# Kernel tuning notes

Measured on AMD Instinct MI355X. Metric: run time of the kernel, lower is better.

The kernel has to match this reference:

```python
import math
import jax, jax.numpy as jnp
import numpy as np

CLUSTER_RATIO1 = 0.0625
CLUSTER_RATIO2 = 0.35
K_LAYER1 = 8
K_LAYER2 = 3


def _dpc_knn(x, cluster_num, k, key):
    """Density-peak clustering with KNN density. x: [B,N,C] -> idx_cluster [B,N]."""
    B, N, C = x.shape
    sq = jnp.sum(x * x, axis=-1)  # [B,N]
    d2 = sq[:, :, None] + sq[:, None, :] - 2.0 * jnp.einsum('bnc,bmc->bnm', x, x)
    dist = jnp.sqrt(jnp.maximum(d2, 0.0)) / jnp.sqrt(jnp.asarray(C, x.dtype))  # cdist / C**0.5
    # k nearest (smallest) distances
    neg_dn, _ = jax.lax.top_k(-dist, k)
    dist_nearest = -neg_dn  # [B,N,k]
    density = jnp.exp(-jnp.mean(dist_nearest ** 2, axis=-1))
    density = density + jax.random.uniform(key, density.shape, dtype=density.dtype) * 1e-6
    mask = (density[:, None, :] > density[:, :, None]).astype(x.dtype)  # [B,N,N]
    dist_max = jnp.max(dist.reshape(B, -1), axis=-1)[:, None, None]
    parent_dist = jnp.min(dist * mask + dist_max * (1.0 - mask), axis=-1)  # [B,N]
    score = parent_dist * density
    _, index_down = jax.lax.top_k(score, cluster_num)  # [B,cluster_num] cluster centers
    # assign each token to nearest center
    dm = jnp.take_along_axis(dist, index_down[:, :, None], axis=1)  # [B,cluster_num,N]
    idx_cluster = jnp.argmin(dm, axis=1)  # [B,N]
    bidx = jnp.arange(B)[:, None]
    idx_cluster = idx_cluster.at[bidx, index_down].set(
        jnp.broadcast_to(jnp.arange(cluster_num)[None, :], index_down.shape))
    return idx_cluster


def _merge_tokens(x, idx_cluster, cluster_num):
    """Weighted (uniform) scatter-mean of tokens into clusters. x: [B,N,C]."""
    B, N, C = x.shape
    flat = (idx_cluster + jnp.arange(B)[:, None] * cluster_num).reshape(-1)  # [B*N]
    ones = jnp.ones((B * N,), x.dtype)
    all_w = jax.ops.segment_sum(ones, flat, num_segments=B * cluster_num) + 1e-6
    norm_w = 1.0 / all_w[flat]  # token_weight == 1
    merged = jax.ops.segment_sum(x.reshape(B * N, C) * norm_w[:, None], flat,
                                 num_segments=B * cluster_num)
    return merged.reshape(B, cluster_num, C)


def _group(meta1, meta2, idx_cluster2, score_w, score_b):
    """Reorder [meta2[v]; members of cluster v from meta1] per cluster, scaled by modulation."""
    T, K1, C = meta1.shape
    K2 = meta2.shape[1]
    modu = jax.nn.softmax(meta2.mean(axis=2) @ score_w.T + score_b, axis=-1)  # [T,K2]
    # composite sort key: (cluster_id, 0 for meta2 center, 1+i for meta1 member i) -> stable grouping
    cid = jnp.concatenate([jnp.broadcast_to(jnp.arange(K2)[None, :], (T, K2)),
                           idx_cluster2], axis=1)  # [T,K2+K1]
    pos = jnp.concatenate([jnp.zeros((T, K2), jnp.int32),
                           jnp.broadcast_to(jnp.arange(1, K1 + 1, dtype=jnp.int32)[None, :], (T, K1))],
                          axis=1)
    sort_key = cid * (K1 + 2) + pos
    order = jnp.argsort(sort_key, axis=1)  # stable; keys are unique anyway
    tokens = jnp.concatenate([meta2, meta1], axis=1)  # [T,K2+K1,C]
    sorted_tokens = jnp.take_along_axis(tokens, order[:, :, None], axis=1)
    sorted_cid = jnp.take_along_axis(cid, order, axis=1)
    scale = jnp.take_along_axis(modu, sorted_cid, axis=1)  # [T,K2+K1]
    return sorted_tokens * scale[:, :, None]


def setup_inputs() -> dict:
    key = jax.random.key(0)
    k1, k2, k3 = jax.random.split(key, 3)
    T, N, C = 128, 256, 1408
    vis_embed = jax.random.normal(k1, (T, N, C), dtype=jnp.float32)
    score_w = jax.random.normal(k2, (6, 6), dtype=jnp.float32) * 0.1
    score_b = jax.random.normal(k3, (6,), dtype=jnp.float32) * 0.1
    return {"vis_embed": vis_embed, "score_w": score_w, "score_b": score_b}


def reference(vis_embed, score_w, score_b):
    T, N, C = vis_embed.shape
    cn1 = max(math.ceil(N * CLUSTER_RATIO1), 1)      # 16
    cn2 = max(math.ceil(cn1 * CLUSTER_RATIO2), 1)    # 6
    nk = jax.random.split(jax.random.key(42), 2)
    idx1 = _dpc_knn(vis_embed, cn1, K_LAYER1, nk[0])
    meta1 = _merge_tokens(vis_embed, idx1, cn1)       # [T,16,C]
    idx2 = _dpc_knn(meta1, cn2, K_LAYER2, nk[1])
    meta2 = _merge_tokens(meta1, idx2, cn2)           # [T,6,C]
    return _group(meta1, meta2, idx2, score_w, score_b)  # [T,22,C]
```

## Files before the change

kernel.cpp:

```cpp
#include <hip/hip_runtime.h>
#include <math.h>

#define T_BATCH 128
#define N_TOK   256
#define C_DIM   1408
#define CN1     16
#define KNN1    8
#define CN2     6
#define KNN2    3
#define NOUT    22
#define LSTR    40

typedef __attribute__((ext_vector_type(4))) short sh4;
typedef __attribute__((ext_vector_type(8))) short sh8;
typedef __attribute__((ext_vector_type(4))) float f32x4;

union frag_u { sh4 h[2]; sh8 v; };

__device__ inline sh8 ld_frag(const short* p) {
    frag_u u;
    u.h[0] = *(const sh4*)p;
    u.h[1] = *(const sh4*)(p + 4);
    return u.v;
}

__device__ inline void split2(float v0, float v1, unsigned& hip, unsigned& lop) {
    unsigned u0 = __float_as_uint(v0);
    unsigned u1 = __float_as_uint(v1);
    hip = (u0 >> 16) | (u1 & 0xFFFF0000u);
    float l0 = v0 - __uint_as_float(u0 & 0xFFFF0000u);
    float l1 = v1 - __uint_as_float(u1 & 0xFFFF0000u);
    unsigned w0 = __float_as_uint(l0);
    unsigned w1 = __float_as_uint(l1);
    w0 = w0 + 0x7FFFu + ((w0 >> 16) & 1u);
    w1 = w1 + 0x7FFFu + ((w1 >> 16) & 1u);
    lop = (w0 >> 16) | (w1 & 0xFFFF0000u);
}

__global__ __launch_bounds__(256, 3) void gemm_dist_mfma(const float* __restrict__ x,
                                                         float* __restrict__ dist) {
    const int t  = blockIdx.z;
    const int i0 = blockIdx.x * 128;
    const int j0 = blockIdx.y * 128;
    const bool diag = (i0 == j0);
    const float* X = x + (size_t)t * N_TOK * C_DIM;

    __shared__ short Ahi[128 * LSTR], Alo[128 * LSTR], Bhi[128 * LSTR], Blo[128 * LSTR];
    __shared__ float nredA[256], nredB[256];
    __shared__ float snA[128], snB[128];

    const int tid  = threadIdx.x;
    const int wave = tid >> 6;
    const int lane = tid & 63;
    const int qr   = wave >> 1;
    const int qc   = wave & 1;
    const int srow = tid >> 1;
    const int scol = (tid & 1) * 16;
    const int fr   = lane & 15;
    const int fq   = lane >> 4;

    const short* BhiS = diag ? Ahi : Bhi;
    const short* BloS = diag ? Alo : Blo;

    f32x4 acc[4][4];
#pragma unroll
    for (int a = 0; a < 4; a++)
#pragma unroll
        for (int b = 0; b < 4; b++) acc[a][b] = (f32x4){0.f, 0.f, 0.f, 0.f};

    const float* Arow = X + (size_t)(i0 + srow) * C_DIM + scol;
    const float* Brow = X + (size_t)(j0 + srow) * C_DIM + scol;
    float nA = 0.f, nB = 0.f;

    for (int k0 = 0; k0 < C_DIM; k0 += 32) {
        float av[16], bv[16];
#pragma unroll
        for (int g = 0; g < 4; g++) {
            float4 a = *(const float4*)(Arow + k0 + g * 4);
            av[g * 4 + 0] = a.x; av[g * 4 + 1] = a.y; av[g * 4 + 2] = a.z; av[g * 4 + 3] = a.w;
        }
#pragma unroll
        for (int e = 0; e < 16; e++) nA += av[e] * av[e];
        if (!diag) {
#pragma unroll
            for (int g = 0; g < 4; g++) {
                float4 b = *(const float4*)(Brow + k0 + g * 4);
                bv[g * 4 + 0] = b.x; bv[g * 4 + 1] = b.y; bv[g * 4 + 2] = b.z; bv[g * 4 + 3] = b.w;
            }
#pragma unroll
            for (int e = 0; e < 16; e++) nB += bv[e] * bv[e];
        }

        unsigned ah[8], al[8], bh[8], bl[8];
#pragma unroll
        for (int p = 0; p < 8; p++) split2(av[2 * p], av[2 * p + 1], ah[p], al[p]);
        if (!diag) {
#pragma unroll
            for (int p = 0; p < 8; p++) split2(bv[2 * p], bv[2 * p + 1], bh[p], bl[p]);
        }
        __syncthreads();
        unsigned* AhiW = (unsigned*)&Ahi[srow * LSTR + scol];
        unsigned* AloW = (unsigned*)&Alo[srow * LSTR + scol];
#pragma unroll
        for (int p = 0; p < 8; p++) { AhiW[p] = ah[p]; AloW[p] = al[p]; }
        if (!diag) {
            unsigned* BhiW = (unsigned*)&Bhi[srow * LSTR + scol];
            unsigned* BloW = (unsigned*)&Blo[srow * LSTR + scol];
#pragma unroll
            for (int p = 0; p < 8; p++) { BhiW[p] = bh[p]; BloW[p] = bl[p]; }
        }
        __syncthreads();

        sh8 fAh[4], fAl[4], fBh[4], fBl[4];
#pragma unroll
        for (int mt = 0; mt < 4; mt++) {
            int ro = (qr * 64 + mt * 16 + fr) * LSTR + fq * 8;
            fAh[mt] = ld_frag(&Ahi[ro]);
            fAl[mt] = ld_frag(&Alo[ro]);
            int co = (qc * 64 + mt * 16 + fr) * LSTR + fq * 8;
            fBh[mt] = ld_frag(&BhiS[co]);
            fBl[mt] = ld_frag(&BloS[co]);
        }
#pragma unroll
        for (int mt = 0; mt < 4; mt++)
#pragma unroll
            for (int nt = 0; nt < 4; nt++) {
                acc[mt][nt] = __builtin_amdgcn_mfma_f32_16x16x32_bf16(fAh[mt], fBh[nt], acc[mt][nt], 0, 0, 0);
                acc[mt][nt] = __builtin_amdgcn_mfma_f32_16x16x32_bf16(fAh[mt], fBl[nt], acc[mt][nt], 0, 0, 0);
                acc[mt][nt] = __builtin_amdgcn_mfma_f32_16x16x32_bf16(fAl[mt], fBh[nt], acc[mt][nt], 0, 0, 0);
            }
    }

    nredA[tid] = nA;
    nredB[tid] = diag ? nA : nB;
    __syncthreads();
    if (tid < 128) {
        snA[tid] = nredA[2 * tid] + nredA[2 * tid + 1];
        snB[tid] = nredB[2 * tid] + nredB[2 * tid + 1];
    }
    __syncthreads();

    const float inv_sqrtC = 1.0f / sqrtf((float)C_DIM);
    float* Dt = dist + (size_t)t * N_TOK * N_TOK;
#pragma unroll
    for (int mt = 0; mt < 4; mt++)
#pragma unroll
        for (int nt = 0; nt < 4; nt++) {
            int jl = qc * 64 + nt * 16 + fr;
            float sqj = snB[jl];
            int jg = j0 + jl;
#pragma unroll
            for (int r = 0; r < 4; r++) {
                int il = qr * 64 + mt * 16 + fq * 4 + r;
                int ig = i0 + il;
                float d2 = snA[il] + sqj - 2.0f * acc[mt][nt][r];
                float v = (ig == jg) ? 0.0f : sqrtf(fmaxf(d2, 0.0f)) * inv_sqrtC;
                Dt[(size_t)ig * N_TOK + jg] = v;
            }
        }
}

__global__ __launch_bounds__(256) void dpc1_fused(const float* __restrict__ dist,
                                                  int* __restrict__ memb,
                                                  int* __restrict__ cntg,
                                                  int* __restrict__ offg) {
    const int t   = blockIdx.x;
    const int tid = threadIdx.x;
    const float* D = dist + (size_t)t * N_TOK * N_TOK;

    __shared__ float dens_s[N_TOK];
    __shared__ float red[N_TOK];
    __shared__ unsigned long long wbest[4];
    __shared__ int centers[CN1];
    __shared__ int bks[N_TOK];
    __shared__ int cnt_s[CN1], off_s[CN1];

    float m[KNN1];
#pragma unroll
    for (int q = 0; q < KNN1; q++) m[q] = 3.4e38f;
    float mx = 0.f;
#pragma unroll 8
    for (int j = 0; j < N_TOK; j++) {
        float d = D[(size_t)j * N_TOK + tid];
        mx = fmaxf(mx, d);
        float xv = d;
#pragma unroll
        for (int q = 0; q < KNN1; q++) {
            float lo = fminf(m[q], xv);
            xv = fmaxf(m[q], xv);
            m[q] = lo;
        }
    }
    float s2 = 0.f;
#pragma unroll
    for (int q = 0; q < KNN1; q++) s2 += m[q] * m[q];
    float dens = expf(-s2 / (float)KNN1);
    dens_s[tid] = dens;
    red[tid] = mx;
    __syncthreads();
#pragma unroll
    for (int s = 128; s > 0; s >>= 1) {
        if (tid < s) red[tid] = fmaxf(red[tid], red[tid + s]);
        __syncthreads();
    }
    float dmax = red[0];

    float pd = dmax;
#pragma unroll 8
    for (int j = 0; j < N_TOK; j++) {
        float d = D[(size_t)j * N_TOK + tid];
        float dj = dens_s[j];
        pd = (dj > dens) ? fminf(pd, d) : pd;
    }
    float score = pd * dens;

    unsigned long long key = ((unsigned long long)__float_as_uint(score) << 32)
                           | (unsigned)(65535 - tid);
    for (int k = 0; k < CN1; k++) {
        unsigned long long mm = key;
#pragma unroll
        for (int off = 32; off > 0; off >>= 1) {
            unsigned long long o = __shfl_xor(mm, off);
            mm = (o > mm) ? o : mm;
        }
        if ((tid & 63) == 0) wbest[tid >> 6] = mm;
        __syncthreads();
        unsigned long long b = wbest[0];
#pragma unroll
        for (int w = 1; w < 4; w++) b = (wbest[w] > b) ? wbest[w] : b;
        int idx = 65535 - (int)(b & 0xFFFFull);
        if (tid == 0) centers[k] = idx;
        if (tid == idx) key = 0;
        __syncthreads();
    }

    float bd = 3.4e38f; int bk = 0;
#pragma unroll
    for (int k = 0; k < CN1; k++) {
        float d = D[(size_t)centers[k] * N_TOK + tid];
        if (d < bd) { bd = d; bk = k; }
    }
#pragma unroll
    for (int k = 0; k < CN1; k++) if (tid == centers[k]) bk = k;

    bks[tid] = bk;
    __syncthreads();
    if (tid < CN1) {
        int c = 0;
        for (int j = 0; j < N_TOK; j++) c += (bks[j] == tid);
        cnt_s[tid] = c;
    }
    __syncthreads();
    if (tid == 0) {
        int o = 0;
        for (int q = 0; q < CN1; q++) { off_s[q] = o; o += cnt_s[q]; }
    }
    __syncthreads();
    int rank = 0;
    for (int j = 0; j < tid; j++) rank += (bks[j] == bk);
    memb[t * N_TOK + off_s[bk] + rank] = tid;
    if (tid < CN1) {
        cntg[t * CN1 + tid] = cnt_s[tid];
        offg[t * CN1 + tid] = off_s[tid];
    }
}

__global__ __launch_bounds__(256) void merge1_kernel(const float* __restrict__ x,
                                                     const int* __restrict__ memb,
                                                     const int* __restrict__ cntg,
                                                     const int* __restrict__ offg,
                                                     float* __restrict__ meta1) {
    const int q   = blockIdx.x;
    const int t   = blockIdx.y;
    const int tid = threadIdx.x;
    const int n    = cntg[t * CN1 + q];
    const int base = t * N_TOK + offg[t * CN1 + q];
    const int c0 = tid, c1 = tid + 256;
    const bool act1 = (c1 < C_DIM / 4);

    float a0x = 0.f, a0y = 0.f, a0z = 0.f, a0w = 0.f;
    float a1x = 0.f, a1y = 0.f, a1z = 0.f, a1w = 0.f;
    for (int m = 0; m < n; m++) {
        int row = memb[base + m];
        const float4* xr = (const float4*)(x + ((size_t)t * N_TOK + row) * C_DIM);
        float4 v0 = xr[c0];
        a0x += v0.x; a0y += v0.y; a0z += v0.z; a0w += v0.w;
        if (act1) {
            float4 v1 = xr[c1];
            a1x += v1.x; a1y += v1.y; a1z += v1.z; a1w += v1.w;
        }
    }
    float w = 1.0f / ((float)n + 1e-6f);
    float4* mr = (float4*)(meta1 + ((size_t)t * CN1 + q) * C_DIM);
    float4 o0; o0.x = a0x * w; o0.y = a0y * w; o0.z = a0z * w; o0.w = a0w * w;
    mr[c0] = o0;
    if (act1) {
        float4 o1; o1.x = a1x * w; o1.y = a1y * w; o1.z = a1z * w; o1.w = a1w * w;
        mr[c1] = o1;
    }
}

__global__ __launch_bounds__(256) void layer2_kernel(const float* __restrict__ meta1,
                                                     const float* __restrict__ score_w,
                                                     const float* __restrict__ score_b,
                                                     float* __restrict__ out) {
    const int t   = blockIdx.x;
    const int tid = threadIdx.x;
    const float* M = meta1 + (size_t)t * CN1 * C_DIM;

    __shared__ float buf[CN1][132];
    __shared__ float d2s[CN1][CN1];
    __shared__ float m2[CN2][C_DIM];
    __shared__ float dens[CN1], scor[CN1], nrm[CN1], rmx[CN1];
    __shared__ int   centers[CN2], idx2s[CN1], cnt2[CN2];
    __shared__ float modu[CN2], msum[CN2];
    __shared__ int   srcRow[NOUT], cidArr[NOUT];
    __shared__ float dmax_sh;

    const int ti = tid >> 4;
    const int tj = tid & 15;

    float acc = 0.f;
    for (int c0 = 0; c0 < C_DIM; c0 += 128) {
        for (int e = tid; e < CN1 * 128; e += 256) {
            int r = e >> 7, c = e & 127;
            buf[r][c] = M[(size_t)r * C_DIM + c0 + c];
        }
        __syncthreads();
#pragma unroll
        for (int cc = 0; cc < 128; cc += 4) {
            float4 a = *(const float4*)&buf[ti][cc];
            float4 b = *(const float4*)&buf[tj][cc];
            acc += a.x * b.x + a.y * b.y + a.z * b.z + a.w * b.w;
        }
        __syncthreads();
    }
    if (ti == tj) nrm[ti] = acc;
    __syncthreads();

    const float inv_sqrtC = 1.0f / sqrtf((float)C_DIM);
    {
        float d2 = nrm[ti] + nrm[tj] - 2.f * acc;
        d2s[ti][tj] = sqrtf(fmaxf(d2, 0.f)) * inv_sqrtC;
    }
    __syncthreads();

    if (tid < CN1) {
        float m0 = 3.4e38f, m1 = 3.4e38f, m2v = 3.4e38f, mx = 0.f;
        for (int j = 0; j < CN1; j++) {
            float d = d2s[tid][j];
            mx = fmaxf(mx, d);
            if (d < m2v) {
                m2v = d;
                if (m2v < m1) { float tmp = m2v; m2v = m1; m1 = tmp; }
                if (m1 < m0)  { float tmp = m1;  m1 = m0;  m0 = tmp; }
            }
        }
        dens[tid] = expf(-(m0 * m0 + m1 * m1 + m2v * m2v) / (float)KNN2);
        rmx[tid] = mx;
    }
    __syncthreads();
    if (tid == 0) {
        float g = 0.f;
        for (int j = 0; j < CN1; j++) g = fmaxf(g, rmx[j]);
        dmax_sh = g;
    }
    __syncthreads();

    if (tid < CN1) {
        float di = dens[tid];
        float pd = dmax_sh;
        for (int j = 0; j < CN1; j++)
            if (dens[j] > di) pd = fminf(pd, d2s[tid][j]);
        scor[tid] = pd * di;
    }
    __syncthreads();

    if (tid == 0) {
        for (int k = 0; k < CN2; k++) {
            float best = -3.4e38f; int bi = 0;
            for (int j = 0; j < CN1; j++)
                if (scor[j] > best) { best = scor[j]; bi = j; }
            centers[k] = bi;
            scor[bi] = -3.4e38f;
        }
    }
    __syncthreads();

    if (tid < CN1) {
        float bd = 3.4e38f; int bk = 0;
#pragma unroll
        for (int k = 0; k < CN2; k++) {
            float d = d2s[centers[k]][tid];
            if (d < bd) { bd = d; bk = k; }
        }
#pragma unroll
        for (int k = 0; k < CN2; k++) if (tid == centers[k]) bk = k;
        idx2s[tid] = bk;
    }
    __syncthreads();

    if (tid == 0) {
        for (int v = 0; v < CN2; v++) cnt2[v] = 0;
        for (int i = 0; i < CN1; i++) cnt2[idx2s[i]]++;
        int slot = 0;
        for (int v = 0; v < CN2; v++) {
            srcRow[slot] = CN1 + v; cidArr[slot] = v; slot++;
            for (int i = 0; i < CN1; i++)
                if (idx2s[i] == v) { srcRow[slot] = i; cidArr[slot] = v; slot++; }
        }
        for (int v = 0; v < CN2; v++) msum[v] = 0.f;
    }
    __syncthreads();

    float ls[CN2] = {0.f, 0.f, 0.f, 0.f, 0.f, 0.f};
    for (int ch = tid; ch < C_DIM; ch += 256) {
        float a6[CN2] = {0.f, 0.f, 0.f, 0.f, 0.f, 0.f};
        for (int r = 0; r < CN1; r++) {
            float v = M[(size_t)r * C_DIM + ch];
            int c = idx2s[r];
#pragma unroll
            for (int q = 0; q < CN2; q++) a6[q] += (c == q) ? v : 0.f;
        }
#pragma unroll
        for (int q = 0; q < CN2; q++) {
            float mv = a6[q] / ((float)cnt2[q] + 1e-6f);
            m2[q][ch] = mv;
            ls[q] += mv;
        }
    }
#pragma unroll
    for (int q = 0; q < CN2; q++) atomicAdd(&msum[q], ls[q]);
    __syncthreads();

    if (tid == 0) {
        float mean[CN2], lg[CN2];
        for (int v = 0; v < CN2; v++) mean[v] = msum[v] / (float)C_DIM;
        float mxl = -3.4e38f;
        for (int u = 0; u < CN2; u++) {
            float s = score_b[u];
            for (int v = 0; v < CN2; v++) s += mean[v] * score_w[u * CN2 + v];
            lg[u] = s;
            mxl = fmaxf(mxl, s);
        }
        float den = 0.f;
        for (int u = 0; u < CN2; u++) { lg[u] = expf(lg[u] - mxl); den += lg[u]; }
        for (int u = 0; u < CN2; u++) modu[u] = lg[u] / den;
    }
    __syncthreads();

    float* ob = out + (size_t)t * NOUT * C_DIM;
    for (int ch = tid; ch < C_DIM; ch += 256) {
#pragma unroll
        for (int s = 0; s < NOUT; s++) {
            int r = srcRow[s];
            float v = (r < CN1) ? M[(size_t)r * C_DIM + ch] : m2[r - CN1][ch];
            ob[(size_t)s * C_DIM + ch] = v * modu[cidArr[s]];
        }
    }
}

extern "C" void kernel_launch(void* const* d_in, const int* in_sizes, int n_in,
                              void* d_out, int out_size, void* d_ws, size_t ws_size,
                              hipStream_t stream) {
    const float* x  = (const float*)d_in[0];
    const float* sw = (const float*)d_in[1];
    const float* sb = (const float*)d_in[2];
    float* out = (float*)d_out;

    float* ws     = (float*)d_ws;
    float* dist   = ws;
    float* meta1  = dist + (size_t)T_BATCH * N_TOK * N_TOK;
    int*   memb   = (int*)(meta1 + (size_t)T_BATCH * CN1 * C_DIM);
    int*   cntg   = memb + (size_t)T_BATCH * N_TOK;
    int*   offg   = cntg + T_BATCH * CN1;

    gemm_dist_mfma<<<dim3(2, 2, T_BATCH), 256, 0, stream>>>(x, dist);
    dpc1_fused<<<T_BATCH, 256, 0, stream>>>(dist, memb, cntg, offg);
    merge1_kernel<<<dim3(CN1, T_BATCH), 256, 0, stream>>>(x, memb, cntg, offg, meta1);
    layer2_kernel<<<T_BATCH, 256, 0, stream>>>(meta1, sw, sb, out);
}
```

Before: 487.5 us.

## Exploit distance symmetry with 64x64 tiles and split KNN density across 512 threads

The distance GEMM moves from 128x128 tiles to 64x64 tiles and computes only the upper-triangular tile pairs (10 per batch), writing each result and its transpose. This cuts redundant MFMA work and gives more blocks for occupancy. The DPC kernel now uses 512 threads, with each half scanning half the rows and using four independent insertion lists for ILP, then merges the partial top-k lists and the parent-distance minima through shared memory. The risks are uncoalesced transposed float4 stores and extra shared memory and merge steps.

```diff
diff --git a/kernel.cpp b/kernel.cpp
--- a/kernel.cpp
+++ b/kernel.cpp
@@ -9,7 +9,7 @@
 #define CN2     6
 #define KNN2    3
 #define NOUT    22
-#define LSTR    40
+#define LS      44
 
 typedef __attribute__((ext_vector_type(4))) short sh4;
 typedef __attribute__((ext_vector_type(8))) short sh8;
@@ -37,185 +37,225 @@
     lop = (w0 >> 16) | (w1 & 0xFFFF0000u);
 }
 
-__global__ __launch_bounds__(256, 3) void gemm_dist_mfma(const float* __restrict__ x,
-                                                         float* __restrict__ dist) {
-    const int t  = blockIdx.z;
-    const int i0 = blockIdx.x * 128;
-    const int j0 = blockIdx.y * 128;
-    const bool diag = (i0 == j0);
+#define INS8(m, v) {                                   \
+    float _x = (v);                                    \
+    _Pragma("unroll")                                  \
+    for (int _q = 0; _q < 8; _q++) {                   \
+        float _lo = fminf(m[_q], _x);                  \
+        _x = fmaxf(m[_q], _x);                         \
+        m[_q] = _lo;                                   \
+    }                                                  \
+}
+
+__global__ __launch_bounds__(256, 4) void gemm_dist_sym(const float* __restrict__ x,
+                                                        float* __restrict__ dist) {
+    const int t = blockIdx.y;
+    const int p = blockIdx.x;
+    const int bi = (p < 4) ? 0 : (p < 7) ? 1 : (p < 9) ? 2 : 3;
+    const int bj = (p < 4) ? p : (p < 7) ? p - 3 : (p < 9) ? p - 5 : 3;
+    const int i0 = bi * 64, j0 = bj * 64;
+    const bool diag = (bi == bj);
     const float* X = x + (size_t)t * N_TOK * C_DIM;
 
-    __shared__ short Ahi[128 * LSTR], Alo[128 * LSTR], Bhi[128 * LSTR], Blo[128 * LSTR];
-    __shared__ float nredA[256], nredB[256];
-    __shared__ float snA[128], snB[128];
+    __shared__ short Ahi[64 * LS], Alo[64 * LS], Bhi[64 * LS], Blo[64 * LS];
+    __shared__ float nred[512];
+    __shared__ float snA[64], snB[64];
 
     const int tid  = threadIdx.x;
     const int wave = tid >> 6;
     const int lane = tid & 63;
     const int qr   = wave >> 1;
     const int qc   = wave & 1;
-    const int srow = tid >> 1;
-    const int scol = (tid & 1) * 16;
+    const int srow = tid >> 2;
+    const int sq   = tid & 3;
     const int fr   = lane & 15;
     const int fq   = lane >> 4;
 
     const short* BhiS = diag ? Ahi : Bhi;
     const short* BloS = diag ? Alo : Blo;
 
-    f32x4 acc[4][4];
-#pragma unroll
-    for (int a = 0; a < 4; a++)
-#pragma unroll
-        for (int b = 0; b < 4; b++) acc[a][b] = (f32x4){0.f, 0.f, 0.f, 0.f};
-
-    const float* Arow = X + (size_t)(i0 + srow) * C_DIM + scol;
-    const float* Brow = X + (size_t)(j0 + srow) * C_DIM + scol;
+    f32x4 acc[2][2];
+#pragma unroll
+    for (int a = 0; a < 2; a++)
+#pragma unroll
+        for (int b = 0; b < 2; b++) acc[a][b] = (f32x4){0.f, 0.f, 0.f, 0.f};
+
+    const float* Arow = X + (size_t)(i0 + srow) * C_DIM + sq * 8;
+    const float* Brow = X + (size_t)(j0 + srow) * C_DIM + sq * 8;
     float nA = 0.f, nB = 0.f;
 
     for (int k0 = 0; k0 < C_DIM; k0 += 32) {
-        float av[16], bv[16];
-#pragma unroll
-        for (int g = 0; g < 4; g++) {
-            float4 a = *(const float4*)(Arow + k0 + g * 4);
-            av[g * 4 + 0] = a.x; av[g * 4 + 1] = a.y; av[g * 4 + 2] = a.z; av[g * 4 + 3] = a.w;
-        }
-#pragma unroll
-        for (int e = 0; e < 16; e++) nA += av[e] * av[e];
+        float av[8], bv[8];
+        float4 a0 = *(const float4*)(Arow + k0);
+        float4 a1 = *(const float4*)(Arow + k0 + 4);
+        av[0] = a0.x; av[1] = a0.y; av[2] = a0.z; av[3] = a0.w;
+        av[4] = a1.x; av[5] = a1.y; av[6] = a1.z; av[7] = a1.w;
+#pragma unroll
+        for (int e = 0; e < 8; e++) nA += av[e] * av[e];
+        unsigned ah[4], al[4], bh[4], bl[4];
+#pragma unroll
+        for (int q = 0; q < 4; q++) split2(av[2 * q], av[2 * q + 1], ah[q], al[q]);
         if (!diag) {
-#pragma unroll
-            for (int g = 0; g < 4; g++) {
-                float4 b = *(const float4*)(Brow + k0 + g * 4);
-                bv[g * 4 + 0] = b.x; bv[g * 4 + 1] = b.y; bv[g * 4 + 2] = b.z; bv[g * 4 + 3] = b.w;
+            float4 b0 = *(const float4*)(Brow + k0);
+            float4 b1 = *(const float4*)(Brow + k0 + 4);
+            bv[0] = b0.x; bv[1] = b0.y; bv[2] = b0.z; bv[3] = b0.w;
+            bv[4] = b1.x; bv[5] = b1.y; bv[6] = b1.z; bv[7] = b1.w;
+#pragma unroll
+            for (int e = 0; e < 8; e++) nB += bv[e] * bv[e];
+#pragma unroll
+            for (int q = 0; q < 4; q++) split2(bv[2 * q], bv[2 * q + 1], bh[q], bl[q]);
+        }
+        __syncthreads();
+        {
+            unsigned* AH = (unsigned*)&Ahi[srow * LS + sq * 8];
+            unsigned* AL = (unsigned*)&Alo[srow * LS + sq * 8];
+#pragma unroll
+            for (int q = 0; q < 4; q++) { AH[q] = ah[q]; AL[q] = al[q]; }
+            if (!diag) {
+                unsigned* BH = (unsigned*)&Bhi[srow * LS + sq * 8];
+                unsigned* BL = (unsigned*)&Blo[srow * LS + sq * 8];
+#pragma unroll
+                for (int q = 0; q < 4; q++) { BH[q] = bh[q]; BL[q] = bl[q]; }
             }
-#pragma unroll
-            for (int e = 0; e < 16; e++) nB += bv[e] * bv[e];
-        }
-
-        unsigned ah[8], al[8], bh[8], bl[8];
-#pragma unroll
-        for (int p = 0; p < 8; p++) split2(av[2 * p], av[2 * p + 1], ah[p], al[p]);
-        if (!diag) {
-#pragma unroll
-            for (int p = 0; p < 8; p++) split2(bv[2 * p], bv[2 * p + 1], bh[p], bl[p]);
-        }
-        __syncthreads();
-        unsigned* AhiW = (unsigned*)&Ahi[srow * LSTR + scol];
-        unsigned* AloW = (unsigned*)&Alo[srow * LSTR + scol];
-#pragma unroll
-        for (int p = 0; p < 8; p++) { AhiW[p] = ah[p]; AloW[p] = al[p]; }
-        if (!diag) {
-            unsigned* BhiW = (unsigned*)&Bhi[srow * LSTR + scol];
-            unsigned* BloW = (unsigned*)&Blo[srow * LSTR + scol];
-#pragma unroll
-            for (int p = 0; p < 8; p++) { BhiW[p] = bh[p]; BloW[p] = bl[p]; }
-        }
-        __syncthreads();
-
-        sh8 fAh[4], fAl[4], fBh[4], fBl[4];
-#pragma unroll
-        for (int mt = 0; mt < 4; mt++) {
-            int ro = (qr * 64 + mt * 16 + fr) * LSTR + fq * 8;
+        }
+        __syncthreads();
+
+        sh8 fAh[2], fAl[2], fBh[2], fBl[2];
+#pragma unroll
+        for (int mt = 0; mt < 2; mt++) {
+            int ro = (qr * 32 + mt * 16 + fr) * LS + fq * 8;
             fAh[mt] = ld_frag(&Ahi[ro]);
             fAl[mt] = ld_frag(&Alo[ro]);
-            int co = (qc * 64 + mt * 16 + fr) * LSTR + fq * 8;
+            int co = (qc * 32 + mt * 16 + fr) * LS + fq * 8;
             fBh[mt] = ld_frag(&BhiS[co]);
             fBl[mt] = ld_frag(&BloS[co]);
         }
 #pragma unroll
-        for (int mt = 0; mt < 4; mt++)
-#pragma unroll
-            for (int nt = 0; nt < 4; nt++) {
+        for (int mt = 0; mt < 2; mt++)
+#pragma unroll
+            for (int nt = 0; nt < 2; nt++) {
                 acc[mt][nt] = __builtin_amdgcn_mfma_f32_16x16x32_bf16(fAh[mt], fBh[nt], acc[mt][nt], 0, 0, 0);
                 acc[mt][nt] = __builtin_amdgcn_mfma_f32_16x16x32_bf16(fAh[mt], fBl[nt], acc[mt][nt], 0, 0, 0);
                 acc[mt][nt] = __builtin_amdgcn_mfma_f32_16x16x32_bf16(fAl[mt], fBh[nt], acc[mt][nt], 0, 0, 0);
             }
     }
 
-    nredA[tid] = nA;
-    nredB[tid] = diag ? nA : nB;
-    __syncthreads();
-    if (tid < 128) {
-        snA[tid] = nredA[2 * tid] + nredA[2 * tid + 1];
-        snB[tid] = nredB[2 * tid] + nredB[2 * tid + 1];
+    nred[tid] = nA;
+    nred[256 + tid] = diag ? nA : nB;
+    __syncthreads();
+    if (tid < 64) {
+        snA[tid] = nred[4 * tid] + nred[4 * tid + 1] + nred[4 * tid + 2] + nred[4 * tid + 3];
+        snB[tid] = nred[256 + 4 * tid] + nred[256 + 4 * tid + 1]
+                 + nred[256 + 4 * tid + 2] + nred[256 + 4 * tid + 3];
     }
     __syncthreads();
 
     const float inv_sqrtC = 1.0f / sqrtf((float)C_DIM);
     float* Dt = dist + (size_t)t * N_TOK * N_TOK;
 #pragma unroll
-    for (int mt = 0; mt < 4; mt++)
-#pragma unroll
-        for (int nt = 0; nt < 4; nt++) {
-            int jl = qc * 64 + nt * 16 + fr;
+    for (int mt = 0; mt < 2; mt++)
+#pragma unroll
+        for (int nt = 0; nt < 2; nt++) {
+            int jl = qc * 32 + nt * 16 + fr;
+            int jg = j0 + jl;
             float sqj = snB[jl];
-            int jg = j0 + jl;
+            int il0 = qr * 32 + mt * 16 + fq * 4;
+            float vv[4];
 #pragma unroll
             for (int r = 0; r < 4; r++) {
-                int il = qr * 64 + mt * 16 + fq * 4 + r;
-                int ig = i0 + il;
-                float d2 = snA[il] + sqj - 2.0f * acc[mt][nt][r];
+                int ig = i0 + il0 + r;
+                float d2 = snA[il0 + r] + sqj - 2.0f * acc[mt][nt][r];
                 float v = (ig == jg) ? 0.0f : sqrtf(fmaxf(d2, 0.0f)) * inv_sqrtC;
                 Dt[(size_t)ig * N_TOK + jg] = v;
+                vv[r] = v;
             }
-        }
-}
-
-__global__ __launch_bounds__(256) void dpc1_fused(const float* __restrict__ dist,
+            if (!diag) {
+                float4 o; o.x = vv[0]; o.y = vv[1]; o.z = vv[2]; o.w = vv[3];
+                *(float4*)&Dt[(size_t)jg * N_TOK + i0 + il0] = o;
+            }
+        }
+}
+
+__global__ __launch_bounds__(512) void dpc1_fused(const float* __restrict__ dist,
                                                   int* __restrict__ memb,
                                                   int* __restrict__ cntg,
                                                   int* __restrict__ offg) {
     const int t   = blockIdx.x;
     const int tid = threadIdx.x;
+    const int col = tid & 255;
+    const int h   = tid >> 8;
     const float* D = dist + (size_t)t * N_TOK * N_TOK;
 
     __shared__ float dens_s[N_TOK];
-    __shared__ float red[N_TOK];
-    __shared__ unsigned long long wbest[4];
+    __shared__ float red[512];
+    __shared__ float lists[KNN1][520];
+    __shared__ unsigned long long wbest[8];
     __shared__ int centers[CN1];
     __shared__ int bks[N_TOK];
     __shared__ int cnt_s[CN1], off_s[CN1];
 
-    float m[KNN1];
-#pragma unroll
-    for (int q = 0; q < KNN1; q++) m[q] = 3.4e38f;
+    float c0[8], c1[8], c2[8], c3[8];
+#pragma unroll
+    for (int q = 0; q < 8; q++) { c0[q] = 3.4e38f; c1[q] = 3.4e38f; c2[q] = 3.4e38f; c3[q] = 3.4e38f; }
     float mx = 0.f;
-#pragma unroll 8
-    for (int j = 0; j < N_TOK; j++) {
-        float d = D[(size_t)j * N_TOK + tid];
-        mx = fmaxf(mx, d);
-        float xv = d;
-#pragma unroll
-        for (int q = 0; q < KNN1; q++) {
-            float lo = fminf(m[q], xv);
-            xv = fmaxf(m[q], xv);
-            m[q] = lo;
-        }
-    }
-    float s2 = 0.f;
-#pragma unroll
-    for (int q = 0; q < KNN1; q++) s2 += m[q] * m[q];
-    float dens = expf(-s2 / (float)KNN1);
-    dens_s[tid] = dens;
+    const float* base = D + (size_t)(h * 128) * N_TOK + col;
+    for (int jj = 0; jj < 128; jj += 4) {
+        float d0 = base[(size_t)(jj + 0) * N_TOK];
+        float d1 = base[(size_t)(jj + 1) * N_TOK];
+        float d2 = base[(size_t)(jj + 2) * N_TOK];
+        float d3 = base[(size_t)(jj + 3) * N_TOK];
+        mx = fmaxf(mx, fmaxf(fmaxf(d0, d1), fmaxf(d2, d3)));
+        INS8(c0, d0); INS8(c1, d1); INS8(c2, d2); INS8(c3, d3);
+    }
+#pragma unroll
+    for (int q = 0; q < 8; q++) { INS8(c0, c1[q]); }
+#pragma unroll
+    for (int q = 0; q < 8; q++) { INS8(c0, c2[q]); }
+#pragma unroll
+    for (int q = 0; q < 8; q++) { INS8(c0, c3[q]); }
+#pragma unroll
+    for (int q = 0; q < 8; q++) lists[q][tid] = c0[q];
     red[tid] = mx;
     __syncthreads();
 #pragma unroll
-    for (int s = 128; s > 0; s >>= 1) {
+    for (int s = 256; s > 0; s >>= 1) {
         if (tid < s) red[tid] = fmaxf(red[tid], red[tid + s]);
         __syncthreads();
     }
-    float dmax = red[0];
-
-    float pd = dmax;
-#pragma unroll 8
-    for (int j = 0; j < N_TOK; j++) {
-        float d = D[(size_t)j * N_TOK + tid];
-        float dj = dens_s[j];
-        pd = (dj > dens) ? fminf(pd, d) : pd;
-    }
-    float score = pd * dens;
-
-    unsigned long long key = ((unsigned long long)__float_as_uint(score) << 32)
-                           | (unsigned)(65535 - tid);
+    const float dmax = red[0];
+    __syncthreads();
+
+    if (h == 0) {
+#pragma unroll
+        for (int q = 0; q < 8; q++) { float v = lists[q][col + 256]; INS8(c0, v); }
+        float s2 = 0.f;
+#pragma unroll
+        for (int q = 0; q < 8; q++) s2 += c0[q] * c0[q];
+        dens_s[col] = expf(-s2 / (float)KNN1);
+    }
+    __syncthreads();
+    const float dens = dens_s[col];
+
+    float p0 = dmax, p1 = dmax, p2 = dmax, p3 = dmax;
+    const float* dsh = dens_s + h * 128;
+    for (int jj = 0; jj < 128; jj += 4) {
+        float d0 = base[(size_t)(jj + 0) * N_TOK];
+        float d1 = base[(size_t)(jj + 1) * N_TOK];
+        float d2 = base[(size_t)(jj + 2) * N_TOK];
+        float d3 = base[(size_t)(jj + 3) * N_TOK];
+        p0 = (dsh[jj + 0] > dens) ? fminf(p0, d0) : p0;
+        p1 = (dsh[jj + 1] > dens) ? fminf(p1, d1) : p1;
+        p2 = (dsh[jj + 2] > dens) ? fminf(p2, d2) : p2;
+        p3 = (dsh[jj + 3] > dens) ? fminf(p3, d3) : p3;
+    }
+    red[tid] = fminf(fminf(p0, p1), fminf(p2, p3));
+    __syncthreads();
+    float score = 0.f;
+    if (h == 0) score = fminf(red[col], red[col + 256]) * dens;
+
+    unsigned long long key = 0;
+    if (h == 0)
+        key = ((unsigned long long)__float_as_uint(score) << 32) | (unsigned)(65535 - col);
     for (int k = 0; k < CN1; k++) {
         unsigned long long mm = key;
 #pragma unroll
@@ -227,23 +267,25 @@
         __syncthreads();
         unsigned long long b = wbest[0];
 #pragma unroll
-        for (int w = 1; w < 4; w++) b = (wbest[w] > b) ? wbest[w] : b;
+        for (int w = 1; w < 8; w++) b = (wbest[w] > b) ? wbest[w] : b;
         int idx = 65535 - (int)(b & 0xFFFFull);
         if (tid == 0) centers[k] = idx;
         if (tid == idx) key = 0;
         __syncthreads();
     }
 
-    float bd = 3.4e38f; int bk = 0;
-#pragma unroll
-    for (int k = 0; k < CN1; k++) {
-        float d = D[(size_t)centers[k] * N_TOK + tid];
-        if (d < bd) { bd = d; bk = k; }
-    }
-#pragma unroll
-    for (int k = 0; k < CN1; k++) if (tid == centers[k]) bk = k;
-
-    bks[tid] = bk;
+    int bk = 0;
+    if (h == 0) {
+        float bd = 3.4e38f;
+#pragma unroll
+        for (int k = 0; k < CN1; k++) {
+            float d = D[(size_t)centers[k] * N_TOK + col];
+            if (d < bd) { bd = d; bk = k; }
+        }
+#pragma unroll
+        for (int k = 0; k < CN1; k++) if (col == centers[k]) bk = k;
+        bks[col] = bk;
+    }
     __syncthreads();
     if (tid < CN1) {
         int c = 0;
@@ -256,9 +298,11 @@
         for (int q = 0; q < CN1; q++) { off_s[q] = o; o += cnt_s[q]; }
     }
     __syncthreads();
-    int rank = 0;
-    for (int j = 0; j < tid; j++) rank += (bks[j] == bk);
-    memb[t * N_TOK + off_s[bk] + rank] = tid;
+    if (h == 0) {
+        int rank = 0;
+        for (int j = 0; j < col; j++) rank += (bks[j] == bk);
+        memb[t * N_TOK + off_s[bk] + rank] = col;
+    }
     if (tid < CN1) {
         cntg[t * CN1 + tid] = cnt_s[tid];
         offg[t * CN1 + tid] = off_s[tid];
@@ -475,8 +519,8 @@
     int*   cntg   = memb + (size_t)T_BATCH * N_TOK;
     int*   offg   = cntg + T_BATCH * CN1;
 
-    gemm_dist_mfma<<<dim3(2, 2, T_BATCH), 256, 0, stream>>>(x, dist);
-    dpc1_fused<<<T_BATCH, 256, 0, stream>>>(dist, memb, cntg, offg);
+    gemm_dist_sym<<<dim3(10, T_BATCH), 256, 0, stream>>>(x, dist);
+    dpc1_fused<<<T_BATCH, 512, 0, stream>>>(dist, memb, cntg, offg);
     merge1_kernel<<<dim3(CN1, T_BATCH), 256, 0, stream>>>(x, memb, cntg, offg, meta1);
     layer2_kernel<<<T_BATCH, 256, 0, stream>>>(meta1, sw, sb, out);
 }
```

After: 443.9 us. -9.0%, faster.
